# Kernel optimization log

Measured on AMD Instinct MI355X. Metric: run time of the kernel, lower is better.

## Reference

```python
import jax, jax.numpy as jnp
import numpy as np

L = 96   # num_layers per GRU stack == seq_len (required by h0 construction in source)
B = 128  # batch
T = 96   # seq_len
D = 3    # input features (x,y,z landmark coords)


def _u(key, shape, s):
    return jax.random.uniform(key, shape, jnp.float32, minval=-s, maxval=s)


def setup_inputs() -> dict:
    key = jax.random.key(0)
    ks = iter(jax.random.split(key, 40))
    inp = {"x": jax.random.normal(next(ks), (B, T, D), jnp.float32)}

    def gru_params(pfx, din, h):
        s = 1.0 / np.sqrt(h).astype(np.float32)  # PyTorch GRU init scale
        inp[pfx + "_wih0"] = _u(next(ks), (3 * h, din), s)   # layer 0 input weights
        inp[pfx + "_bih0"] = _u(next(ks), (3 * h,), s)
        inp[pfx + "_whh0"] = _u(next(ks), (3 * h, h), s)
        inp[pfx + "_bhh0"] = _u(next(ks), (3 * h,), s)
        inp[pfx + "_wih"] = _u(next(ks), (L - 1, 3 * h, h), s)  # layers 1..L-1 (input dim == h)
        inp[pfx + "_bih"] = _u(next(ks), (L - 1, 3 * h), s)
        inp[pfx + "_whh"] = _u(next(ks), (L - 1, 3 * h, h), s)
        inp[pfx + "_bhh"] = _u(next(ks), (L - 1, 3 * h), s)

    gru_params("g1", D, 64)
    gru_params("g2", 64, 128)
    gru_params("g3", 128, 64)

    inp["d1_w"] = _u(next(ks), (64, 64), 1.0 / 8)
    inp["d1_b"] = _u(next(ks), (64,), 1.0 / 8)
    inp["d2_w"] = _u(next(ks), (32, 64), 1.0 / 8)
    inp["d2_b"] = _u(next(ks), (32,), 1.0 / 8)
    inp["d3_w"] = _u(next(ks), (250, 32), 1.0 / np.sqrt(32).astype(np.float32))
    inp["d3_b"] = _u(next(ks), (250,), 1.0 / np.sqrt(32).astype(np.float32))
    return inp


def _gru_layer(x, wih, bih, whh, bhh):
    # x: [B,T,Din]; wih: [3H,Din]; whh: [3H,H]. PyTorch gate order: r,z,n.
    h = whh.shape[1]
    xg = jnp.einsum('btd,gd->btg', x, wih) + bih  # precompute input gates [B,T,3H]

    def step(hprev, xg_t):
        hg = hprev @ whh.T + bhh
        xr, xz, xn = jnp.split(xg_t, 3, axis=-1)
        hr, hz, hn = jnp.split(hg, 3, axis=-1)
        r = jax.nn.sigmoid(xr + hr)
        z = jax.nn.sigmoid(xz + hz)
        n = jnp.tanh(xn + r * hn)
        hnew = (1.0 - z) * n + z * hprev
        return hnew, hnew

    h0 = jnp.zeros((x.shape[0], h), x.dtype)
    _, ys = jax.lax.scan(step, h0, jnp.swapaxes(xg, 0, 1))  # scan over time
    return jnp.swapaxes(ys, 0, 1)  # [B,T,H]


def _gru_stack(x, wih0, bih0, whh0, bhh0, wih, bih, whh, bhh):
    y = _gru_layer(x, wih0, bih0, whh0, bhh0)

    def body(y, p):
        return _gru_layer(y, p[0], p[1], p[2], p[3]), None

    y, _ = jax.lax.scan(body, y, (wih, bih, whh, bhh))  # scan over layers 1..L-1
    return y


def reference(x,
              g1_wih0, g1_bih0, g1_whh0, g1_bhh0, g1_wih, g1_bih, g1_whh, g1_bhh,
              g2_wih0, g2_bih0, g2_whh0, g2_bhh0, g2_wih, g2_bih, g2_whh, g2_bhh,
              g3_wih0, g3_bih0, g3_whh0, g3_bhh0, g3_wih, g3_bih, g3_whh, g3_bhh,
              d1_w, d1_b, d2_w, d2_b, d3_w, d3_b):
    y = _gru_stack(x, g1_wih0, g1_bih0, g1_whh0, g1_bhh0, g1_wih, g1_bih, g1_whh, g1_bhh)
    y = _gru_stack(y, g2_wih0, g2_bih0, g2_whh0, g2_bhh0, g2_wih, g2_bih, g2_whh, g2_bhh)
    y = _gru_stack(y, g3_wih0, g3_bih0, g3_whh0, g3_bhh0, g3_wih, g3_bih, g3_whh, g3_bhh)
    h = y[:, -1, :]  # last timestep [B,64]
    h = jax.nn.relu(h @ d1_w.T + d1_b)
    h = jax.nn.relu(h @ d2_w.T + d2_b)
    return jax.nn.relu(h @ d3_w.T + d3_b)  # [B,250]
```

## Files before the change

kernel.cpp:

```cpp
#include <hip/hip_runtime.h>


#define TPB 512
#define DRING 4
#define FS 64
#define PROBE_A 0x51CAFE77
#define PROBE_B 0x2B2B2B2B

typedef float vf4 __attribute__((ext_vector_type(4)));

__device__ __forceinline__ float sigmoid_f(float x) { return 1.0f / (1.0f + __expf(-x)); }
__device__ __forceinline__ float tanh_f(float x)    { return 1.0f - 2.0f / (__expf(2.0f * x) + 1.0f); }

__device__ __forceinline__ int cp_load(const int* p) {
    return __hip_atomic_load(p, __ATOMIC_RELAXED, __HIP_MEMORY_SCOPE_AGENT);
}
__device__ __forceinline__ void cp_store(int* p, int v) {
    __hip_atomic_store(p, v, __ATOMIC_RELAXED, __HIP_MEMORY_SCOPE_AGENT);
}
__device__ __forceinline__ int cp_poll_nz(const int* p) {
    int v;
    while (!(v = cp_load(p))) __builtin_amdgcn_s_sleep(8);
    return v;
}

__device__ __forceinline__ void vmwait0() { asm volatile("s_waitcnt vmcnt(0)" ::: "memory"); }
__device__ __forceinline__ int ld_l2_b32_wait(const int* p) {
    int r;
    asm volatile("global_load_dword %0, %1, off sc0\n\t"
                 "s_waitcnt vmcnt(0)"
                 : "=v"(r) : "v"(p) : "memory");
    return r;
}
__device__ __forceinline__ void st_l2_b32(int* p, int v) {
    asm volatile("global_store_dword %0, %1, off sc0" :: "v"(p), "v"(v) : "memory");
}
__device__ __forceinline__ void st_l2_f4(float* p, float4 v) {
    vf4 w; w[0] = v.x; w[1] = v.y; w[2] = v.z; w[3] = v.w;
    asm volatile("global_store_dwordx4 %0, %1, off sc0" :: "v"(p), "v"(w) : "memory");
}
__device__ __forceinline__ void ld_l2_2xf4(const float* p0, const float* p1,
                                           vf4& a, vf4& b) {
    asm volatile("global_load_dwordx4 %0, %2, off sc0\n\t"
                 "global_load_dwordx4 %1, %3, off sc0\n\t"
                 "s_waitcnt vmcnt(0)"
                 : "=&v"(a), "=&v"(b)
                 : "v"(p0), "v"(p1)
                 : "memory");
}
__device__ __forceinline__ void ld_l2_4xf4(const float* p0, const float* p1,
                                           const float* p2, const float* p3,
                                           vf4& a, vf4& b, vf4& c, vf4& d) {
    asm volatile("global_load_dwordx4 %0, %4, off sc0\n\t"
                 "global_load_dwordx4 %1, %5, off sc0\n\t"
                 "global_load_dwordx4 %2, %6, off sc0\n\t"
                 "global_load_dwordx4 %3, %7, off sc0\n\t"
                 "s_waitcnt vmcnt(0)"
                 : "=&v"(a), "=&v"(b), "=&v"(c), "=&v"(d)
                 : "v"(p0), "v"(p1), "v"(p2), "v"(p3)
                 : "memory");
}

__device__ __forceinline__ void st_cp_f4(float* p, float4 v) {
    vf4 w; w[0] = v.x; w[1] = v.y; w[2] = v.z; w[3] = v.w;
    asm volatile("global_store_dwordx4 %0, %1, off sc0 sc1" :: "v"(p), "v"(w) : "memory");
}
__device__ __forceinline__ void ld_cp_2xf4(const float* p0, const float* p1,
                                           vf4& a, vf4& b) {
    asm volatile("global_load_dwordx4 %0, %2, off sc0 sc1\n\t"
                 "global_load_dwordx4 %1, %3, off sc0 sc1\n\t"
                 "s_waitcnt vmcnt(0)"
                 : "=&v"(a), "=&v"(b)
                 : "v"(p0), "v"(p1)
                 : "memory");
}
__device__ __forceinline__ void ld_cp_4xf4(const float* p0, const float* p1,
                                           const float* p2, const float* p3,
                                           vf4& a, vf4& b, vf4& c, vf4& d) {
    asm volatile("global_load_dwordx4 %0, %4, off sc0 sc1\n\t"
                 "global_load_dwordx4 %1, %5, off sc0 sc1\n\t"
                 "global_load_dwordx4 %2, %6, off sc0 sc1\n\t"
                 "global_load_dwordx4 %3, %7, off sc0 sc1\n\t"
                 "s_waitcnt vmcnt(0)"
                 : "=&v"(a), "=&v"(b), "=&v"(c), "=&v"(d)
                 : "v"(p0), "v"(p1), "v"(p2), "v"(p3)
                 : "memory");
}

__device__ __forceinline__ void wait_flag(int* fp, int tgt, bool fast) {
    if (fast) { while (ld_l2_b32_wait(fp) < tgt) __builtin_amdgcn_s_sleep(1); }
    else      { while (cp_load(fp) < tgt)        __builtin_amdgcn_s_sleep(2); }
}

struct PassArgs {
    const float* wih0; const float* bih0; const float* whh0; const float* bhh0;
    const float* wihA; const float* bihA; const float* whhA; const float* bhhA;
    int firstLayer;
    int NL;
    const float* seqIn;
    long seqTs;
    float* seqOut;
    float* hFinal;
    float* rings;
    int* done;
    int* prb;
    const float* xg;
    const int* prevDone;
    int prevBase;
    int prevN;
    int cpSeqOut;
};

template<int STACK>
__device__ void pass_body(const PassArgs& A, int l, int part, int tid,
                          float* wt_hh, float* wt_ih, float* atile, float* hbuf)
{
    constexpr int NG    = (STACK == 2) ? 96 : 192;
    constexpr int KH    = (STACK == 2) ? 128 : 64;
    constexpr int KI    = (STACK == 2) ? 128 : 64;
    constexpr int PARTS = (STACK == 2) ? 4 : 2;
    constexpr int JS    = NG / 3;
    constexpr int NGG   = NG / 6;
    constexpr int BGN   = TPB / NGG;
    constexpr int WROW  = NGG * 12;
    constexpr int XGT   = (STACK == 2) ? 384 * 128 : 192 * 128;

    const int rb = l * PARTS + part;
    const int gl = A.firstLayer + l;
    const bool useXG = (A.xg != nullptr);

    const int gg = tid / BGN;
    const int bg = tid % BGN;
    const int jl0 = 2 * gg, jl1 = 2 * gg + 1;
    const int b0 = 4 * bg;

    const float *wih, *bih, *whh, *bhh;
    if (gl == 0) { wih = A.wih0; bih = A.bih0; whh = A.whh0; bhh = A.bhh0; }
    else {
        const int wsz = (STACK == 2) ? 384 * 128 : 192 * 64;
        const int bs  = (STACK == 2) ? 384 : 192;
        wih = A.wihA + (size_t)(gl - 1) * wsz; bih = A.bihA + (size_t)(gl - 1) * bs;
        whh = A.whhA + (size_t)(gl - 1) * wsz; bhh = A.bhhA + (size_t)(gl - 1) * bs;
    }
    const int din = (gl == 0) ? ((STACK == 1) ? 3 : ((STACK == 2) ? 64 : 128))
                              : ((STACK == 2) ? 128 : 64);

    auto grow = [&](int r) -> int {
        if (STACK == 2) return (r >> 5) * 128 + 32 * part + (r & 31);
        return r;
    };

    for (int i = tid; i < NG * KH; i += TPB) {
        int r = i / KH, k = i - r * KH;
        int g = r / JS, j = r - g * JS;
        wt_hh[(k >> 1) * WROW + (j >> 1) * 12 + (k & 1) * 6 + g * 2 + (j & 1)]
            = whh[(size_t)grow(r) * KH + k];
    }
    if (l > 0 || !useXG) {
        for (int i = tid; i < NG * KI; i += TPB) {
            int r = i / KI, k = i - r * KI;
            int g = r / JS, j = r - g * JS;
            wt_ih[(k >> 1) * WROW + (j >> 1) * 12 + (k & 1) * 6 + g * 2 + (j & 1)]
                = (k < din) ? wih[(size_t)grow(r) * din + k] : 0.0f;
        }
    }

    float bR[2], bZ[2], bNH[2], bNI[2];
#pragma unroll
    for (int jj = 0; jj < 2; ++jj) {
        int jl = jl0 + jj;
        bR[jj]  = bhh[grow(jl)]          + bih[grow(jl)];
        bZ[jj]  = bhh[grow(JS + jl)]     + bih[grow(JS + jl)];
        bNH[jj] = bhh[grow(2 * JS + jl)];
        bNI[jj] = bih[grow(2 * JS + jl)];
    }

    float hprev[2][4];
#pragma unroll
    for (int jj = 0; jj < 2; ++jj)
#pragma unroll
        for (int bb = 0; bb < 4; ++bb) hprev[jj][bb] = 0.0f;

    bool f_in = false, f_out = false, f_fl_self = false, f_fl_par = false, f_fl_child = false;
    {
        int* hsk = (int*)atile;
        const int NL = A.NL;
        if (STACK != 2) {
            if (tid == 0 && l < NL - 1) {
                int* rg = A.prb + (size_t)rb * FS;
                cp_store(rg, PROBE_A); vmwait0();
                (void)ld_l2_b32_wait(rg);
                cp_store(rg, PROBE_B); vmwait0();
                cp_store(rg + 1, 1);
            }
            if (tid == 1 && l > 0) {
                int* rg = A.prb + (size_t)((l - 1) * PARTS + part) * FS;
                (void)cp_poll_nz(rg + 1);
                int v = ld_l2_b32_wait(rg);
                cp_store(rg + 2, (v == PROBE_A) ? 2 : 1);
            }
            if (tid >= 8 && tid < 12) {
                int j = l - 2 + (tid - 8);
                hsk[tid - 8] = (j >= 0 && j < NL - 1)
                    ? cp_poll_nz(A.prb + (size_t)(j * PARTS + part) * FS + 2) : 0;
            }
        } else {
            if (part == 0 && tid < 4 && (tid > 0 || l < NL - 1)) {
                int* rg = A.prb + (size_t)(l * 4 + tid) * FS;
                cp_store(rg, PROBE_A); vmwait0();
                (void)ld_l2_b32_wait(rg);
                cp_store(rg, PROBE_B); vmwait0();
                cp_store(rg + 1, 1);
            }
            if (tid == 4 && (part != 0 || l > 0)) {
                int* rg = (part != 0) ? A.prb + (size_t)(l * 4 + part) * FS
                                      : A.prb + (size_t)((l - 1) * 4) * FS;
                (void)cp_poll_nz(rg + 1);
                int v = ld_l2_b32_wait(rg);
                cp_store(rg + 2, (v == PROBE_A) ? 2 : 1);
            }
            if (tid >= 8 && tid < 28) {
                int q = tid - 8, r = q >> 2, p = q & 3;
                int a = l - 2 + r;
                bool valid = (a >= 0 && a < NL) && (p > 0 || a < NL - 1);
                hsk[q] = valid ? cp_poll_nz(A.prb + (size_t)(a * 4 + p) * FS + 2) : 0;
            }
        }
        __syncthreads();
        if (STACK != 2) {
            const int NLl = A.NL;
            bool pp0 = hsk[0] == 2, pp1 = hsk[1] == 2, pp2 = hsk[2] == 2, pp3 = hsk[3] == 2;
            f_in       = (l > 0) && pp1;
            f_out      = (l == NLl - 1) || pp2;
            f_fl_self  = (l == 0 || pp1) && (l == NLl - 1 || pp2);
            f_fl_par   = (l > 0) && pp1 && (l < 2 || pp0);
            f_fl_child = (l < NLl - 1) && pp2 && (l + 2 >= NLl || pp3);
        } else {
            const int NLl = A.NL;
            bool S[5], T[4];
#pragma unroll
            for (int r = 0; r < 5; ++r)
                S[r] = hsk[r * 4 + 1] == 2 && hsk[r * 4 + 2] == 2 && hsk[r * 4 + 3] == 2;
#pragma unroll
            for (int r = 0; r < 4; ++r) T[r] = hsk[r * 4 + 0] == 2;
            f_out      = S[2] && (l == NLl - 1 || (S[3] && T[2]));
            f_in       = (l > 0) && S[1] && S[2] && T[1];
            f_fl_self  = S[2] && (l == 0 || (S[1] && T[1])) && (l == NLl - 1 || (S[3] && T[2]));
            f_fl_par   = (l > 0) && S[1] && S[2] && T[1] && (l < 2 || (S[0] && T[0]));
            f_fl_child = (l < NLl - 1) && S[2] && S[3] && T[2] && (l + 2 >= NLl || (S[4] && T[3]));
        }
        __syncthreads();
    }

    auto gemmP = [&](const float* wt, const float* at, int astride,
                     float (&accR)[2][4], float (&accZ)[2][4], float (&accN)[2][4]) {
#pragma unroll 2
        for (int k2 = 0; k2 < 32; ++k2) {
            const float* wr = wt + k2 * WROW + gg * 12;
            vf4 q0 = *(const vf4*)(wr);
            vf4 q1 = *(const vf4*)(wr + 4);
            vf4 q2 = *(const vf4*)(wr + 8);
            const float* ar = at + (2 * k2) * astride + b0;
            float4 a0v = *(const float4*)(ar);
            float4 a1v = *(const float4*)(ar + astride);
            float a0[4] = {a0v.x, a0v.y, a0v.z, a0v.w};
            float a1[4] = {a1v.x, a1v.y, a1v.z, a1v.w};
#pragma unroll
            for (int bb = 0; bb < 4; ++bb) {
                accR[0][bb] += q0.x * a0[bb];  accR[1][bb] += q0.y * a0[bb];
                accZ[0][bb] += q0.z * a0[bb];  accZ[1][bb] += q0.w * a0[bb];
                accN[0][bb] += q1.x * a0[bb];  accN[1][bb] += q1.y * a0[bb];
                accR[0][bb] += q1.z * a1[bb];  accR[1][bb] += q1.w * a1[bb];
                accZ[0][bb] += q2.x * a1[bb];  accZ[1][bb] += q2.y * a1[bb];
                accN[0][bb] += q2.z * a1[bb];  accN[1][bb] += q2.w * a1[bb];
            }
        }
    };

    auto stage2 = [&](int baseBlk, int slotT, int kt, bool fast) {
        const float* p[4];
#pragma unroll
        for (int q = 0; q < 4; ++q) {
            int u4 = tid + q * TPB, r = u4 >> 5, c4 = u4 & 31, kk = kt * 64 + r;
            p[q] = A.rings + ((size_t)(baseBlk + (kk >> 5)) * DRING + slotT) * 4096
                           + (kk & 31) * 128 + 4 * c4;
        }
        vf4 ta, tb, tc, td;
        if (fast) ld_l2_4xf4(p[0], p[1], p[2], p[3], ta, tb, tc, td);
        else      ld_cp_4xf4(p[0], p[1], p[2], p[3], ta, tb, tc, td);
        {
            int u4, r, c4;
            u4 = tid;           r = u4 >> 5; c4 = u4 & 31; *(vf4*)&atile[r * 128 + 4 * c4] = ta;
            u4 = tid + TPB;     r = u4 >> 5; c4 = u4 & 31; *(vf4*)&atile[r * 128 + 4 * c4] = tb;
            u4 = tid + 2 * TPB; r = u4 >> 5; c4 = u4 & 31; *(vf4*)&atile[r * 128 + 4 * c4] = tc;
            u4 = tid + 3 * TPB; r = u4 >> 5; c4 = u4 & 31; *(vf4*)&atile[r * 128 + 4 * c4] = td;
        }
    };

    for (int t = 0; t < 96; ++t) {
        float accR[2][4] = {}, accZ[2][4] = {}, accNH[2][4] = {}, accNI[2][4] = {};

        if (STACK != 2) {
            if (t > 0) gemmP(wt_hh, hbuf, 64, accR, accZ, accNH);

            if (tid < 8) {
                int grp = tid >> 2, idx = tid & 3;
                int* fp = nullptr; int tgt = 0; bool fm = false;
                if (grp == 0) { if (l > 0 && idx == part)
                                { fp = &A.done[((l - 1) * PARTS + idx) * FS]; tgt = t + 1; fm = f_fl_par; } }
                else          { if (t >= DRING && l < A.NL - 1 && idx == part)
                                { fp = &A.done[((l + 1) * PARTS + idx) * FS]; tgt = t - DRING + 1; fm = f_fl_child; } }
                if (fp) wait_flag(fp, tgt, fm);
            }
            __syncthreads();

            if (l == 0) {
                const float* xgp = A.xg + (size_t)t * XGT + 64 * part + b0;
                auto xgacc = [&](int row, float (&acc)[4]) {
                    float4 xv = *(const float4*)&xgp[(size_t)row * 128];
                    acc[0] += xv.x; acc[1] += xv.y; acc[2] += xv.z; acc[3] += xv.w;
                };
                xgacc(jl0, accR[0]);            xgacc(jl1, accR[1]);
                xgacc(JS + jl0, accZ[0]);       xgacc(JS + jl1, accZ[1]);
                xgacc(2 * JS + jl0, accNI[0]);  xgacc(2 * JS + jl1, accNI[1]);
            } else {
                const float* slot = A.rings + ((size_t)((l - 1) * PARTS + part) * DRING + (t & 3)) * 4096;
                vf4 ta, tb;
                if (f_in) ld_l2_2xf4(slot + 4 * tid, slot + 4 * (tid + TPB), ta, tb);
                else      ld_cp_2xf4(slot + 4 * tid, slot + 4 * (tid + TPB), ta, tb);
                *(vf4*)&atile[4 * tid] = ta;
                *(vf4*)&atile[4 * (tid + TPB)] = tb;
                __syncthreads();
                gemmP(wt_ih, atile, 64, accR, accZ, accNI);
            }
        } else {
            if (t > 0) {
                if (tid < 4 && tid != part)
                    wait_flag(&A.done[(l * 4 + tid) * FS], t, f_fl_self);
                __syncthreads();
                for (int kt = 0; kt < 2; ++kt) {
                    if (kt) __syncthreads();
                    stage2(l * 4, (t - 1) & 3, kt, f_out);
                    __syncthreads();
                    gemmP(wt_hh + kt * 32 * WROW, atile, 128, accR, accZ, accNH);
                }
            }

            if (tid < 8) {
                int grp = tid >> 2, idx = tid & 3;
                int* fp = nullptr; int tgt = 0; bool fm = false;
                if (grp == 0) {
                    if (l > 0) { fp = &A.done[((l - 1) * 4 + idx) * FS]; tgt = t + 1; fm = f_fl_par; }
                    else if (A.prevDone && idx < A.prevN)
                         { fp = (int*)&A.prevDone[(A.prevBase + idx) * FS]; tgt = t + 1; fm = false; }
                }
                else { if (t >= DRING && l < A.NL - 1)
                       { fp = &A.done[((l + 1) * 4 + idx) * FS]; tgt = t - DRING + 1; fm = f_fl_child; } }
                if (fp) wait_flag(fp, tgt, fm);
            }
            __syncthreads();

            if (l == 0 && useXG) {
                const float* xgp = A.xg + (size_t)t * XGT + b0;
                auto xgacc = [&](int row, float (&acc)[4]) {
                    float4 xv = *(const float4*)&xgp[(size_t)row * 128];
                    acc[0] += xv.x; acc[1] += xv.y; acc[2] += xv.z; acc[3] += xv.w;
                };
                xgacc(grow(jl0), accR[0]);            xgacc(grow(jl1), accR[1]);
                xgacc(grow(JS + jl0), accZ[0]);       xgacc(grow(JS + jl1), accZ[1]);
                xgacc(grow(2 * JS + jl0), accNI[0]);  xgacc(grow(2 * JS + jl1), accNI[1]);
            } else {
                const int nkt = (l == 0 && A.firstLayer == 0) ? 1 : 2;
                for (int kt = 0; kt < nkt; ++kt) {
                    if (kt) __syncthreads();
                    if (l == 0) {
                        const float* src = A.seqIn + (size_t)t * A.seqTs + (size_t)kt * 64 * 128;
                        if (A.prevDone) {
                            vf4 a, b, c, d;
                            ld_cp_4xf4(src + 4 * tid, src + 4 * (tid + TPB),
                                       src + 4 * (tid + 2 * TPB), src + 4 * (tid + 3 * TPB),
                                       a, b, c, d);
                            *(vf4*)&atile[4 * tid] = a;
                            *(vf4*)&atile[4 * (tid + TPB)] = b;
                            *(vf4*)&atile[4 * (tid + 2 * TPB)] = c;
                            *(vf4*)&atile[4 * (tid + 3 * TPB)] = d;
                        } else {
                            for (int i = tid; i < 2048; i += TPB)
                                *(float4*)&atile[4 * i] = *(const float4*)(src + 4 * i);
                        }
                    } else {
                        stage2((l - 1) * 4, t & 3, kt, f_in);
                    }
                    __syncthreads();
                    gemmP(wt_ih + kt * 32 * WROW, atile, 128, accR, accZ, accNI);
                }
            }
        }

        float4 hv[2];
#pragma unroll
        for (int jj = 0; jj < 2; ++jj) {
            float* hp = (float*)&hv[jj];
#pragma unroll
            for (int bb = 0; bb < 4; ++bb) {
                float r = sigmoid_f(accR[jj][bb] + bR[jj]);
                float z = sigmoid_f(accZ[jj][bb] + bZ[jj]);
                float n = tanh_f(accNI[jj][bb] + bNI[jj] + r * (accNH[jj][bb] + bNH[jj]));
                float h = (1.0f - z) * n + z * hprev[jj][bb];
                hprev[jj][bb] = h;
                hp[bb] = h;
            }
        }
        float* slot = A.rings + ((size_t)rb * DRING + (t & 3)) * 4096;
        if (STACK == 2) {
            if (f_out) {
                st_l2_f4(&slot[jl0 * 128 + b0], hv[0]);
                st_l2_f4(&slot[jl1 * 128 + b0], hv[1]);
            } else {
                st_cp_f4(&slot[jl0 * 128 + b0], hv[0]);
                st_cp_f4(&slot[jl1 * 128 + b0], hv[1]);
            }
            if (A.seqOut && l == A.NL - 1) {
                float* o0 = &A.seqOut[(size_t)t * 16384 + (32 * part + jl0) * 128 + b0];
                float* o1 = &A.seqOut[(size_t)t * 16384 + (32 * part + jl1) * 128 + b0];
                if (A.cpSeqOut) { st_cp_f4(o0, hv[0]); st_cp_f4(o1, hv[1]); }
                else            { *(float4*)o0 = hv[0]; *(float4*)o1 = hv[1]; }
            }
        } else {
            if (f_out) {
                st_l2_f4(&slot[jl0 * 64 + b0], hv[0]);
                st_l2_f4(&slot[jl1 * 64 + b0], hv[1]);
            } else {
                st_cp_f4(&slot[jl0 * 64 + b0], hv[0]);
                st_cp_f4(&slot[jl1 * 64 + b0], hv[1]);
            }
            *(float4*)&hbuf[jl0 * 64 + b0] = hv[0];
            *(float4*)&hbuf[jl1 * 64 + b0] = hv[1];
            if (A.seqOut && l == A.NL - 1) {
                float* o0 = &A.seqOut[(size_t)t * 16384 + jl0 * 128 + 64 * part + b0];
                float* o1 = &A.seqOut[(size_t)t * 16384 + jl1 * 128 + 64 * part + b0];
                if (A.cpSeqOut) { st_cp_f4(o0, hv[0]); st_cp_f4(o1, hv[1]); }
                else            { *(float4*)o0 = hv[0]; *(float4*)o1 = hv[1]; }
            }
            if (STACK == 3 && l == A.NL - 1 && t == 95 && A.hFinal) {
                *(float4*)&A.hFinal[jl0 * 128 + 64 * part + b0] = hv[0];
                *(float4*)&A.hFinal[jl1 * 128 + 64 * part + b0] = hv[1];
            }
        }
        vmwait0();
        __syncthreads();
        if (tid == 0) {
            if (f_fl_self) st_l2_b32(&A.done[rb * FS], t + 1);
            else           cp_store(&A.done[rb * FS], t + 1);
        }
    }
}

__global__ __launch_bounds__(TPB, 2) void fused_kernel(PassArgs P1, PassArgs P2, PassArgs P3)
{
    __shared__ __align__(16) float wt_hh[12288];
    __shared__ __align__(16) float wt_ih[12288];
    __shared__ __align__(16) float atile[8192];
    __shared__ __align__(16) float hbuf[4096];

    const int tid  = threadIdx.x;
    const int bidx = blockIdx.x;

    {
        int l = 12 * (bidx & 7) + ((bidx >> 3) >> 1), part = (bidx >> 3) & 1;
        pass_body<1>(P1, l, part, tid, wt_hh, wt_ih, atile, hbuf);
    }
    __syncthreads();
    {
        int l = 6 * (bidx & 7) + ((bidx >> 3) >> 2), part = (bidx >> 3) & 3;
        pass_body<2>(P2, l, part, tid, wt_hh, wt_ih, atile, hbuf);
        __syncthreads();
        pass_body<2>(P3, l, part, tid, wt_hh, wt_ih, atile, hbuf);
    }
}

__global__ __launch_bounds__(TPB, 2) void pass4_kernel(PassArgs A)
{
    __shared__ __align__(16) float wt_hh[12288];
    __shared__ __align__(16) float wt_ih[12288];
    __shared__ __align__(16) float atile[4096];
    __shared__ __align__(16) float hbuf[4096];

    const int tid  = threadIdx.x;
    const int bidx = blockIdx.x;
    int l = 12 * (bidx & 7) + ((bidx >> 3) >> 1), part = (bidx >> 3) & 1;
    pass_body<3>(A, l, part, tid, wt_hh, wt_ih, atile, hbuf);
}

__global__ __launch_bounds__(256) void xg_kernel(const float* __restrict__ W,
    const float* __restrict__ X, float* __restrict__ XG,
    int NGtot, int din, long xts)
{
    __shared__ float xs[16384];
    const int t = blockIdx.x, r0 = blockIdx.y * 64, tid = threadIdx.x;
    for (int i = tid; i < din * 128; i += 256)
        xs[i] = X[(size_t)t * xts + i];
    __syncthreads();
    const int rr = tid >> 2, bq = tid & 3;
    const int r = r0 + rr;
    vf4 acc[8];
#pragma unroll
    for (int j = 0; j < 8; ++j) acc[j] = (vf4){0.f, 0.f, 0.f, 0.f};
    for (int k = 0; k < din; ++k) {
        float w = W[(size_t)r * din + k];
        const float* xr = &xs[k * 128 + bq * 32];
#pragma unroll
        for (int j = 0; j < 8; ++j) {
            vf4 xv = *(const vf4*)(xr + 4 * j);
            acc[j] += w * xv;
        }
    }
    float* out = &XG[((size_t)t * NGtot + r) * 128 + bq * 32];
#pragma unroll
    for (int j = 0; j < 8; ++j) *(vf4*)(out + 4 * j) = acc[j];
}

__global__ void xprep_kernel(const float* __restrict__ x, float* __restrict__ seqA)
{
    int i = blockIdx.x * 256 + threadIdx.x;
    if (i < 128 * 96 * 3) {
        int b = i / 288, r = i - b * 288;
        int t = r / 3, k = r - 3 * t;
        seqA[(size_t)t * 8192 + k * 128 + b] = x[i];
    }
}

__global__ __launch_bounds__(256) void head_kernel(
    const float* __restrict__ hF,
    const float* __restrict__ d1w, const float* __restrict__ d1b,
    const float* __restrict__ d2w, const float* __restrict__ d2b,
    const float* __restrict__ d3w, const float* __restrict__ d3b,
    float* __restrict__ out)
{
    const int b = blockIdx.x, tid = threadIdx.x;
    __shared__ float h1[64], h2[32];
    if (tid < 64) {
        float s = d1b[tid];
        for (int k = 0; k < 64; ++k) s += d1w[tid * 64 + k] * hF[k * 128 + b];
        h1[tid] = fmaxf(s, 0.0f);
    }
    __syncthreads();
    if (tid < 32) {
        float s = d2b[tid];
        for (int k = 0; k < 64; ++k) s += d2w[tid * 64 + k] * h1[k];
        h2[tid] = fmaxf(s, 0.0f);
    }
    __syncthreads();
    if (tid < 250) {
        float s = d3b[tid];
        for (int k = 0; k < 32; ++k) s += d3w[tid * 32 + k] * h2[k];
        out[b * 250 + tid] = fmaxf(s, 0.0f);
    }
}

extern "C" void kernel_launch(void* const* d_in, const int* in_sizes, int n_in,
                              void* d_out, int out_size, void* d_ws, size_t ws_size,
                              hipStream_t stream)
{
    const float* x       = (const float*)d_in[0];
    const float* g1_wih0 = (const float*)d_in[1];  const float* g1_bih0 = (const float*)d_in[2];
    const float* g1_whh0 = (const float*)d_in[3];  const float* g1_bhh0 = (const float*)d_in[4];
    const float* g1_wih  = (const float*)d_in[5];  const float* g1_bih  = (const float*)d_in[6];
    const float* g1_whh  = (const float*)d_in[7];  const float* g1_bhh  = (const float*)d_in[8];
    const float* g2_wih0 = (const float*)d_in[9];  const float* g2_bih0 = (const float*)d_in[10];
    const float* g2_whh0 = (const float*)d_in[11]; const float* g2_bhh0 = (const float*)d_in[12];
    const float* g2_wih  = (const float*)d_in[13]; const float* g2_bih  = (const float*)d_in[14];
    const float* g2_whh  = (const float*)d_in[15]; const float* g2_bhh  = (const float*)d_in[16];
    const float* g3_wih0 = (const float*)d_in[17]; const float* g3_bih0 = (const float*)d_in[18];
    const float* g3_whh0 = (const float*)d_in[19]; const float* g3_bhh0 = (const float*)d_in[20];
    const float* g3_wih  = (const float*)d_in[21]; const float* g3_bih  = (const float*)d_in[22];
    const float* g3_whh  = (const float*)d_in[23]; const float* g3_bhh  = (const float*)d_in[24];
    const float* d1w = (const float*)d_in[25]; const float* d1b = (const float*)d_in[26];
    const float* d2w = (const float*)d_in[27]; const float* d2b = (const float*)d_in[28];
    const float* d3w = (const float*)d_in[29]; const float* d3b = (const float*)d_in[30];

    float* wsf = (float*)d_ws;
    const size_t RINGS = (size_t)192 * DRING * 4096;
    const size_t B1SZ  = (size_t)96 * 128 * 128;
    const size_t SEQA  = (size_t)96 * 64 * 128;
    const int    SLOTN = 192 * FS;
    float* rings1 = wsf;
    float* rings2 = rings1 + RINGS;
    float* rings3 = rings2 + RINGS;
    float* B1     = rings3 + RINGS;
    float* B2     = B1 + B1SZ;
    float* seqA   = B2 + B1SZ;
    float* hFinal = seqA + SEQA;
    int*   flags  = (int*)(hFinal + 8192);
    int*   prb    = flags + (size_t)4 * SLOTN;
    float* XG     = (float*)(prb + (size_t)4 * SLOTN);

    size_t zero_bytes = (B1SZ * 2 + SEQA + 8192) * sizeof(float)
                      + (size_t)8 * SLOTN * sizeof(int);
    (void)hipMemsetAsync(B1, 0, zero_bytes, stream);

    xprep_kernel<<<dim3(144), dim3(256), 0, stream>>>(x, seqA);

    xg_kernel<<<dim3(96, 3), dim3(256), 0, stream>>>(g1_wih0, seqA, XG, 192, 3, 8192);

    PassArgs P1 = {g1_wih0, g1_bih0, g1_whh0, g1_bhh0, g1_wih, g1_bih, g1_whh, g1_bhh,
                   0, 96, seqA, 8192, B1, nullptr, rings1, flags + 0 * SLOTN, prb + 0 * SLOTN,
                   XG, nullptr, 0, 0, 1};
    PassArgs P2 = {g2_wih0, g2_bih0, g2_whh0, g2_bhh0, g2_wih, g2_bih, g2_whh, g2_bhh,
                   0, 48, B1, 16384, B2, nullptr, rings2, flags + 1 * SLOTN, prb + 1 * SLOTN,
                   nullptr, flags + 0 * SLOTN, 95 * 2, 2, 1};
    PassArgs P3 = {g2_wih0, g2_bih0, g2_whh0, g2_bhh0, g2_wih, g2_bih, g2_whh, g2_bhh,
                   48, 48, B2, 16384, B1, nullptr, rings3, flags + 2 * SLOTN, prb + 2 * SLOTN,
                   nullptr, flags + 1 * SLOTN, 47 * 4, 4, 0};
    fused_kernel<<<dim3(192), dim3(TPB), 0, stream>>>(P1, P2, P3);

    xg_kernel<<<dim3(96, 3), dim3(256), 0, stream>>>(g3_wih0, B1, XG, 192, 128, 16384);

    PassArgs P4 = {g3_wih0, g3_bih0, g3_whh0, g3_bhh0, g3_wih, g3_bih, g3_whh, g3_bhh,
                   0, 96, B1, 16384, nullptr, hFinal, rings1, flags + 3 * SLOTN, prb + 3 * SLOTN,
                   XG, nullptr, 0, 0, 0};
    pass4_kernel<<<dim3(192), dim3(TPB), 0, stream>>>(P4);

    head_kernel<<<dim3(128), dim3(256), 0, stream>>>(hFinal, d1w, d1b, d2w, d2b, d3w, d3b,
                                                     (float*)d_out);
}
```

Measured before the change: 8.108 ms.

## Fuse third GRU stack into persistent kernel with streamed layer-0 input projection

Stack 3 now runs inside the persistent fused kernel after stack 2, so the separate xg_kernel and pass4_kernel launches go away. Layer 0 of stack 3 waits on the previous pass's per-timestep done flags and computes its input projection inline. It does this in two 64-wide K halves, reloading half of wih into shared memory every timestep, instead of reading a precomputed XG buffer. The aim is to pipeline stack 3 behind stack 2 and drop a kernel-launch barrier. The cost is repeated weight restaging and extra syncs on the critical path of layer 0, plus a fourth ring buffer in the workspace.

```diff
diff --git a/kernel.cpp b/kernel.cpp
--- a/kernel.cpp
+++ b/kernel.cpp
@@ -144,6 +144,7 @@
     }
     const int din = (gl == 0) ? ((STACK == 1) ? 3 : ((STACK == 2) ? 64 : 128))
                               : ((STACK == 2) ? 128 : 64);
+    const bool dualIH = (STACK != 2) && (l == 0) && !useXG;
 
     auto grow = [&](int r) -> int {
         if (STACK == 2) return (r >> 5) * 128 + 32 * part + (r & 31);
@@ -297,6 +298,19 @@
         }
     };
 
+    auto stageDual = [&](int t, int kt) {
+        const float* srcb = A.seqIn + (size_t)t * A.seqTs + (size_t)kt * 64 * 128 + 64 * part;
+        int i0 = tid, i1 = tid + TPB;
+        const float* p0 = srcb + (i0 >> 4) * 128 + (i0 & 15) * 4;
+        const float* p1 = srcb + (i1 >> 4) * 128 + (i1 & 15) * 4;
+        vf4 a, b;
+        ld_cp_2xf4(p0, p1, a, b);
+        *(vf4*)&atile[(i0 >> 4) * 64 + (i0 & 15) * 4] = a;
+        *(vf4*)&atile[(i1 >> 4) * 64 + (i1 & 15) * 4] = b;
+    };
+
+    int res = 0;
+
     for (int t = 0; t < 96; ++t) {
         float accR[2][4] = {}, accZ[2][4] = {}, accNH[2][4] = {}, accNI[2][4] = {};
 
@@ -306,15 +320,19 @@
             if (tid < 8) {
                 int grp = tid >> 2, idx = tid & 3;
                 int* fp = nullptr; int tgt = 0; bool fm = false;
-                if (grp == 0) { if (l > 0 && idx == part)
-                                { fp = &A.done[((l - 1) * PARTS + idx) * FS]; tgt = t + 1; fm = f_fl_par; } }
-                else          { if (t >= DRING && l < A.NL - 1 && idx == part)
-                                { fp = &A.done[((l + 1) * PARTS + idx) * FS]; tgt = t - DRING + 1; fm = f_fl_child; } }
+                if (grp == 0) {
+                    if (l > 0 && idx == part)
+                        { fp = &A.done[((l - 1) * PARTS + idx) * FS]; tgt = t + 1; fm = f_fl_par; }
+                    else if (l == 0 && A.prevDone && idx < A.prevN)
+                        { fp = (int*)&A.prevDone[(A.prevBase + idx) * FS]; tgt = t + 1; fm = false; }
+                }
+                else { if (t >= DRING && l < A.NL - 1 && idx == part)
+                       { fp = &A.done[((l + 1) * PARTS + idx) * FS]; tgt = t - DRING + 1; fm = f_fl_child; } }
                 if (fp) wait_flag(fp, tgt, fm);
             }
             __syncthreads();
 
-            if (l == 0) {
+            if (l == 0 && useXG) {
                 const float* xgp = A.xg + (size_t)t * XGT + 64 * part + b0;
                 auto xgacc = [&](int row, float (&acc)[4]) {
                     float4 xv = *(const float4*)&xgp[(size_t)row * 128];
@@ -323,6 +341,24 @@
                 xgacc(jl0, accR[0]);            xgacc(jl1, accR[1]);
                 xgacc(JS + jl0, accZ[0]);       xgacc(JS + jl1, accZ[1]);
                 xgacc(2 * JS + jl0, accNI[0]);  xgacc(2 * JS + jl1, accNI[1]);
+            } else if (dualIH) {
+                stageDual(t, res);
+                __syncthreads();
+                gemmP(wt_ih, atile, 64, accR, accZ, accNI);
+                __syncthreads();
+                {
+                    int kt2 = res ^ 1;
+                    for (int i = tid; i < 192 * 64; i += TPB) {
+                        int r = i >> 6, k = i & 63;
+                        int g = r / JS, j = r - g * JS;
+                        wt_ih[(k >> 1) * WROW + (j >> 1) * 12 + (k & 1) * 6 + g * 2 + (j & 1)]
+                            = wih[(size_t)r * 128 + kt2 * 64 + k];
+                    }
+                    stageDual(t, kt2);
+                }
+                __syncthreads();
+                gemmP(wt_ih, atile, 64, accR, accZ, accNI);
+                res ^= 1;
             } else {
                 const float* slot = A.rings + ((size_t)((l - 1) * PARTS + part) * DRING + (t & 3)) * 4096;
                 vf4 ta, tb;
@@ -456,7 +492,8 @@
     }
 }
 
-__global__ __launch_bounds__(TPB, 2) void fused_kernel(PassArgs P1, PassArgs P2, PassArgs P3)
+__global__ __launch_bounds__(TPB, 2) void fused_kernel(PassArgs P1, PassArgs P2,
+                                                       PassArgs P3, PassArgs P4)
 {
     __shared__ __align__(16) float wt_hh[12288];
     __shared__ __align__(16) float wt_ih[12288];
@@ -465,31 +502,16 @@
 
     const int tid  = threadIdx.x;
     const int bidx = blockIdx.x;
-
-    {
-        int l = 12 * (bidx & 7) + ((bidx >> 3) >> 1), part = (bidx >> 3) & 1;
-        pass_body<1>(P1, l, part, tid, wt_hh, wt_ih, atile, hbuf);
-    }
+    const int l13  = 12 * (bidx & 7) + ((bidx >> 3) >> 1), p13 = (bidx >> 3) & 1;
+    const int l2   = 6 * (bidx & 7) + ((bidx >> 3) >> 2),  p2  = (bidx >> 3) & 3;
+
+    pass_body<1>(P1, l13, p13, tid, wt_hh, wt_ih, atile, hbuf);
     __syncthreads();
-    {
-        int l = 6 * (bidx & 7) + ((bidx >> 3) >> 2), part = (bidx >> 3) & 3;
-        pass_body<2>(P2, l, part, tid, wt_hh, wt_ih, atile, hbuf);
-        __syncthreads();
-        pass_body<2>(P3, l, part, tid, wt_hh, wt_ih, atile, hbuf);
-    }
-}
-
-__global__ __launch_bounds__(TPB, 2) void pass4_kernel(PassArgs A)
-{
-    __shared__ __align__(16) float wt_hh[12288];
-    __shared__ __align__(16) float wt_ih[12288];
-    __shared__ __align__(16) float atile[4096];
-    __shared__ __align__(16) float hbuf[4096];
-
-    const int tid  = threadIdx.x;
-    const int bidx = blockIdx.x;
-    int l = 12 * (bidx & 7) + ((bidx >> 3) >> 1), part = (bidx >> 3) & 1;
-    pass_body<3>(A, l, part, tid, wt_hh, wt_ih, atile, hbuf);
+    pass_body<2>(P2, l2, p2, tid, wt_hh, wt_ih, atile, hbuf);
+    __syncthreads();
+    pass_body<2>(P3, l2, p2, tid, wt_hh, wt_ih, atile, hbuf);
+    __syncthreads();
+    pass_body<3>(P4, l13, p13, tid, wt_hh, wt_ih, atile, hbuf);
 }
 
 __global__ __launch_bounds__(256) void xg_kernel(const float* __restrict__ W,
@@ -587,7 +609,8 @@
     float* rings1 = wsf;
     float* rings2 = rings1 + RINGS;
     float* rings3 = rings2 + RINGS;
-    float* B1     = rings3 + RINGS;
+    float* rings4 = rings3 + RINGS;
+    float* B1     = rings4 + RINGS;
     float* B2     = B1 + B1SZ;
     float* seqA   = B2 + B1SZ;
     float* hFinal = seqA + SEQA;
@@ -611,15 +634,11 @@
                    nullptr, flags + 0 * SLOTN, 95 * 2, 2, 1};
     PassArgs P3 = {g2_wih0, g2_bih0, g2_whh0, g2_bhh0, g2_wih, g2_bih, g2_whh, g2_bhh,
                    48, 48, B2, 16384, B1, nullptr, rings3, flags + 2 * SLOTN, prb + 2 * SLOTN,
-                   nullptr, flags + 1 * SLOTN, 47 * 4, 4, 0};
-    fused_kernel<<<dim3(192), dim3(TPB), 0, stream>>>(P1, P2, P3);
-
-    xg_kernel<<<dim3(96, 3), dim3(256), 0, stream>>>(g3_wih0, B1, XG, 192, 128, 16384);
-
+                   nullptr, flags + 1 * SLOTN, 47 * 4, 4, 1};
     PassArgs P4 = {g3_wih0, g3_bih0, g3_whh0, g3_bhh0, g3_wih, g3_bih, g3_whh, g3_bhh,
-                   0, 96, B1, 16384, nullptr, hFinal, rings1, flags + 3 * SLOTN, prb + 3 * SLOTN,
-                   XG, nullptr, 0, 0, 0};
-    pass4_kernel<<<dim3(192), dim3(TPB), 0, stream>>>(P4);
+                   0, 96, B1, 16384, nullptr, hFinal, rings4, flags + 3 * SLOTN, prb + 3 * SLOTN,
+                   nullptr, flags + 2 * SLOTN, 47 * 4, 4, 0};
+    fused_kernel<<<dim3(192), dim3(TPB), 0, stream>>>(P1, P2, P3, P4);
 
     head_kernel<<<dim3(128), dim3(256), 0, stream>>>(hFinal, d1w, d1b, d2w, d2b, d3w, d3b,
                                                      (float*)d_out);
```

Result: no change. 8.004 ms (-1.3%).
